# Performance work log

Measured on AMD Instinct MI355X. Metric: run time of the kernel, lower is better.

## Reference

```python
import jax, jax.numpy as jnp
import numpy as np

N_GRAPHS = 8192
NODES_PER = 32
H = 128
E = 524288
N = N_GRAPHS * NODES_PER


def setup_inputs() -> dict:
    key = jax.random.key(0)
    ks = jax.random.split(key, 20)
    feat = jax.random.normal(ks[0], (N, H), jnp.float32)
    # edges constrained within each session graph
    gid_e = jax.random.randint(ks[1], (E,), 0, N_GRAPHS)
    src = (gid_e * NODES_PER + jax.random.randint(ks[2], (E,), 0, NODES_PER)).astype(jnp.int32)
    dst = (gid_e * NODES_PER + jax.random.randint(ks[3], (E,), 0, NODES_PER)).astype(jnp.int32)
    cnt = jax.random.uniform(ks[4], (N,), jnp.float32, 1.0, 4.0)
    segment_ids = jnp.repeat(jnp.arange(N_GRAPHS, dtype=jnp.int32), NODES_PER)
    last_nodes = (jnp.arange(N_GRAPHS, dtype=jnp.int32) + 1) * NODES_PER - 1
    s = 1.0 / np.sqrt(H)
    u = lambda k, shape: jax.random.uniform(k, shape, jnp.float32, -s, s)
    return {
        'feat': feat, 'cnt': cnt,
        'W_in': u(ks[5], (H, H)), 'b_in': u(ks[6], (H,)),
        'W_og': u(ks[7], (H, H)), 'b_og': u(ks[8], (H,)),
        'W_ih': u(ks[9], (3 * H, 2 * H)), 'b_ih': u(ks[10], (3 * H,)),
        'W_hh': u(ks[11], (3 * H, H)), 'b_hh': u(ks[12], (3 * H,)),
        'W_u': u(ks[13], (H, H)),
        'W_v': u(ks[14], (H, H)), 'b_v': u(ks[15], (H,)),
        'w_e': u(ks[16], (H,)),
        'src': src, 'dst': dst, 'segment_ids': segment_ids, 'last_nodes': last_nodes,
    }


def reference(feat, cnt, W_in, b_in, W_og, b_og, W_ih, b_ih, W_hh, b_hh,
              W_u, W_v, b_v, w_e, src, dst, segment_ids, last_nodes):
    n = feat.shape[0]
    ones = jnp.ones(src.shape, jnp.float32)
    deg_in = jax.ops.segment_sum(ones, dst, num_segments=n)   # in-degree per node
    deg_out = jax.ops.segment_sum(ones, src, num_segments=n)  # out-degree per node
    # GGNN propagate (num_steps=1): copy_u_mean on g and on reversed g
    feat_in = feat @ W_in.T + b_in
    feat_out = feat @ W_og.T + b_og
    a_in = jax.ops.segment_sum(feat_in[src], dst, num_segments=n) / jnp.maximum(deg_in, 1.0)[:, None]
    a_out = jax.ops.segment_sum(feat_out[dst], src, num_segments=n) / jnp.maximum(deg_out, 1.0)[:, None]
    a = jnp.concatenate([a_in, a_out], axis=1)  # [N, 2H]
    # torch GRUCell
    gi = a @ W_ih.T + b_ih
    gh = feat @ W_hh.T + b_hh
    i_r, i_z, i_n = jnp.split(gi, 3, axis=1)
    h_r, h_z, h_n = jnp.split(gh, 3, axis=1)
    r = jax.nn.sigmoid(i_r + h_r)
    z = jax.nn.sigmoid(i_z + h_z)
    ng = jnp.tanh(i_n + r * h_n)
    hn = (1.0 - z) * ng + z * feat  # [N, H]
    # AttentionReadout
    feat_u = hn @ W_u.T
    feat_v = hn[last_nodes] @ W_v.T + b_v           # [B, H]
    e = jax.nn.sigmoid(feat_u + feat_v[segment_ids]) @ w_e  # [N]
    alpha = e * cnt
    ct_g = jax.ops.segment_sum(hn * alpha[:, None], segment_ids, num_segments=N_GRAPHS)
    ct_l = hn[last_nodes]
    return jnp.concatenate([ct_g, ct_l], axis=1)  # [B, 2H]
```

## Files before the change

### kernel.cpp

```cpp
#include <hip/hip_runtime.h>


#define NG    8192
#define NODES 32
#define HDIM  128
#define NEDGE 524288
#define NCONV 214272

typedef __bf16 bf16;
typedef __bf16 bf16x8 __attribute__((ext_vector_type(8)));
typedef float  f32x4  __attribute__((ext_vector_type(4)));
typedef unsigned int u32;
typedef unsigned char u8;

__device__ __forceinline__ f32x4 mfma16(bf16x8 a, bf16x8 b, f32x4 c) {
    return __builtin_amdgcn_mfma_f32_16x16x32_bf16(a, b, c, 0, 0, 0);
}

__device__ __forceinline__ float sigmoidf_(float x) { return 1.f / (1.f + __expf(-x)); }
__device__ __forceinline__ float tanhf_(float x) { return 1.f - 2.f / (__expf(2.f * x) + 1.f); }

__global__ __launch_bounds__(256) void k_prep(
        const u32* __restrict__ featw, u32* __restrict__ adjw,
        bf16* __restrict__ conv, u32* __restrict__ flagout,
        const void* t0, const void* t1, const void* t2,  const void* t3,
        const void* t4, const void* t5, const void* t6,  const void* t7,
        const void* t8, const void* t9, const void* t10, const void* t11) {
    const int b = blockIdx.x, tid = threadIdx.x;
    if (b < 2048) {
        int i = b * 1024 + tid * 4;
        *(uint4*)(adjw + i) = make_uint4(0u, 0u, 0u, 0u);
        return;
    }
    __shared__ int s_isf32;
    if (tid == 0) s_isf32 = 0;
    __syncthreads();
    {
        u32 hit = 0;
#pragma unroll
        for (int k = 0; k < 16; ++k) {
            u32 x = featw[tid * 16 + k];
            hit |= (((x >> 7) & 0xFFu) == 0xFFu) ? 1u : 0u;
        }
        if (hit) s_isf32 = 1;
    }
    __syncthreads();
    const bool isf32 = s_isf32 != 0;
    if (b == 2048 && tid == 0) *flagout = isf32 ? 1u : 0u;

    int e0 = (b - 2048) * 2048 + tid * 8;
    if (e0 >= NCONV) return;
    const int cnts[12] = {16384, 128, 16384, 128, 98304, 384, 49152, 384,
                          16384, 16384, 128, 128};
    int t = 0, base = 0;
    while (e0 >= base + cnts[t]) { base += cnts[t]; ++t; }
    int off = e0 - base;
    const void* sp;
    switch (t) {
        case 0: sp = t0; break; case 1: sp = t1; break;
        case 2: sp = t2; break; case 3: sp = t3; break;
        case 4: sp = t4; break; case 5: sp = t5; break;
        case 6: sp = t6; break; case 7: sp = t7; break;
        case 8: sp = t8; break; case 9: sp = t9; break;
        case 10: sp = t10; break; default: sp = t11; break;
    }
    if (isf32) {
        const float4* s = (const float4*)sp + (off >> 2);
        float4 a = s[0], bb = s[1];
        bf16x8 v;
        v[0] = (bf16)a.x;  v[1] = (bf16)a.y;  v[2] = (bf16)a.z;  v[3] = (bf16)a.w;
        v[4] = (bf16)bb.x; v[5] = (bf16)bb.y; v[6] = (bf16)bb.z; v[7] = (bf16)bb.w;
        *(bf16x8*)(conv + e0) = v;
    } else {
        *(uint4*)(conv + e0) = ((const uint4*)sp)[off >> 3];
    }
}

__global__ __launch_bounds__(256) void k_fuse(
        const bf16* __restrict__ W_in, const bf16* __restrict__ b_in,
        const bf16* __restrict__ W_og, const bf16* __restrict__ b_og,
        const bf16* __restrict__ W_ih, const bf16* __restrict__ b_ih,
        bf16* __restrict__ u_t, float* __restrict__ bw_in,
        float* __restrict__ bw_og) {
    const int jt = blockIdx.x;
    const int tid = threadIdx.x;
    const int wave = tid >> 6, lane = tid & 63, q = lane >> 4, c = lane & 15;
#pragma unroll 1
    for (int k2 = 0; k2 < 4; ++k2) {
        int kt = wave * 4 + k2;
        bool og = kt >= 8;
        const bf16* Wsrc = og ? W_og : W_in;
        int kcol = (kt & 7) * 16 + c;
        int mo = og ? 128 : 0;
        f32x4 acc = {0, 0, 0, 0};
#pragma unroll 1
        for (int t = 0; t < 4; ++t) {
            bf16x8 a = *(const bf16x8*)(W_ih + (jt * 16 + c) * 256 + mo + 32 * t + 8 * q);
            bf16x8 b;
#pragma unroll
            for (int jj = 0; jj < 8; ++jj)
                b[jj] = Wsrc[(32 * t + 8 * q + jj) * 128 + kcol];
            acc = mfma16(a, b, acc);
        }
#pragma unroll
        for (int r = 0; r < 4; ++r)
            u_t[(size_t)(jt * 16 + q * 4 + r) * 256 + kt * 16 + c] = (bf16)acc[r];
    }
    {
        int jj = tid >> 4, mm = tid & 15;
        int j = jt * 16 + jj;
        float si = 0.f, so = 0.f;
#pragma unroll
        for (int i = 0; i < 8; ++i) {
            int m = mm * 8 + i;
            si += (float)b_in[m] * (float)W_ih[j * 256 + m];
            so += (float)b_og[m] * (float)W_ih[j * 256 + 128 + m];
        }
        for (int m = 1; m < 16; m <<= 1) {
            si += __shfl_xor(si, m);
            so += __shfl_xor(so, m);
        }
        if (mm == 0) { bw_in[j] = si; bw_og[j] = so; }
    }
}

__global__ __launch_bounds__(256) void k_adj(const int* __restrict__ src,
                                             const int* __restrict__ dst,
                                             u32* __restrict__ adj) {
    int e = blockIdx.x * 256 + threadIdx.x;
    int s = src[e], d = dst[e];
    int g = s >> 5;
    u32 bidx = ((u32)g << 10) | ((u32)(d & 31) << 5) | (u32)(s & 31);
    atomicAdd(&adj[bidx >> 2], 1u << (8 * (bidx & 3)));
}

__global__ __launch_bounds__(512, 4) void k_mono(
        const void* __restrict__ featv, const void* __restrict__ cntv,
        const bf16* __restrict__ u_t,  const bf16* __restrict__ b_ih,
        const bf16* __restrict__ W_hh, const bf16* __restrict__ b_hh,
        const bf16* __restrict__ W_u,  const bf16* __restrict__ W_v,
        const bf16* __restrict__ b_v,  const bf16* __restrict__ w_e,
        const float* __restrict__ bw_in, const float* __restrict__ bw_og,
        const int* __restrict__ last_nodes, const u8* __restrict__ adj8,
        const u32* __restrict__ flag, float* __restrict__ out) {
    const int g2   = blockIdx.x;
    const int tid  = threadIdx.x;
    const int wave = tid >> 6, lane = tid & 63, q = lane >> 4, c = lane & 15;
    const bool isf32 = (*flag) != 0u;
    const int col  = wave * 16 + c;

    const int SF = 136;
    const int SC = 264;
    const int SA = 40;
    __shared__ __align__(16) bf16 s_feat[64 * 136];
    __shared__ __align__(16) bf16 s_fc  [64 * 264];
    __shared__ __align__(16) bf16 s_adjb[64 * 40];
    __shared__ __align__(16) bf16 s_adjT[64 * 40];
    __shared__ u32   s_adjw[512];
    __shared__ float s_invin[64], s_invout[64];
    __shared__ float s_din[64], s_dout[64];
    __shared__ float s_e[64], s_alpha[64];
    float* s_fv = (float*)s_adjw;

    if (isf32) {
        const float4* fp = (const float4*)((const float*)featv + (size_t)g2 * 8192);
        for (int ch = tid; ch < 2048; ch += 512) {
            float4 v = fp[ch];
            int row = ch >> 5, off = (ch & 31) * 4;
            bf16* dp = s_feat + row * SF + off;
            dp[0] = (bf16)v.x; dp[1] = (bf16)v.y; dp[2] = (bf16)v.z; dp[3] = (bf16)v.w;
        }
    } else {
        const uint4* fp = (const uint4*)((const bf16*)featv + (size_t)g2 * 8192);
        for (int ch = tid; ch < 1024; ch += 512) {
            int row = ch >> 4, off = (ch & 15) * 8;
            *(uint4*)(s_feat + row * SF + off) = fp[ch];
        }
    }
    s_adjw[tid] = ((const u32*)(adj8 + (size_t)g2 * 2048))[tid];
    if (tid < 64) s_e[tid] = 0.f;
    __syncthreads();

    {
        u32 w = s_adjw[tid];
        int vrow = tid >> 3;
        int grp  = tid >> 8;
        int vloc = vrow & 31;
        int u0 = (tid & 7) * 4;
#pragma unroll
        for (int j = 0; j < 4; ++j) {
            float cv = (float)((w >> (8 * j)) & 0xFFu);
            s_adjb[vrow * SA + u0 + j] = (bf16)cv;
            s_adjT[(grp * 32 + u0 + j) * SA + vloc] = (bf16)cv;
        }
    }
    if (tid < 64) {
        u32 s = 0;
        for (int i = 0; i < 8; ++i) {
            u32 w = s_adjw[tid * 8 + i];
            s += (w & 0xFF) + ((w >> 8) & 0xFF) + ((w >> 16) & 0xFF) + (w >> 24);
        }
        s_invin[tid] = 1.f / fmaxf((float)s, 1.f);
        s_din[tid] = (s > 0) ? 1.f : 0.f;
    } else if (tid < 128) {
        int uu = tid - 64; int grp = uu >> 5; int ul = uu & 31; u32 s = 0;
        for (int v = 0; v < 32; ++v)
            s += (s_adjw[grp * 256 + v * 8 + (ul >> 2)] >> (8 * (ul & 3))) & 0xFF;
        s_invout[uu] = 1.f / fmaxf((float)s, 1.f);
        s_dout[uu] = (s > 0) ? 1.f : 0.f;
    }
    f32x4 hnp[4] = {{0,0,0,0},{0,0,0,0},{0,0,0,0},{0,0,0,0}};
    {
        const bf16* Vp = W_hh + (256 + col) * HDIM;
#pragma unroll 1
        for (int t = 0; t < 4; ++t) {
            bf16x8 b = *(const bf16x8*)(Vp + 32 * t + 8 * q);
#pragma unroll
            for (int fr = 0; fr < 4; ++fr) {
                bf16x8 a = *(const bf16x8*)(s_feat + (fr * 16 + c) * SF + 32 * t + 8 * q);
                hnp[fr] = mfma16(a, b, hnp[fr]);
            }
        }
        float bh = (float)b_hh[256 + col];
#pragma unroll
        for (int fr = 0; fr < 4; ++fr)
#pragma unroll
            for (int r = 0; r < 4; ++r) hnp[fr][r] += bh;
    }
    __syncthreads();

#pragma unroll 1
    for (int kk = 0; kk < 2; ++kk) {
        int ct = wave * 2 + kk;
        int colb = (ct & 7) * 16;
        const bf16* Ab = (ct < 8) ? s_adjb : s_adjT;
        const float* inv = (ct < 8) ? s_invin : s_invout;
        bf16x8 bA, bB;
        const bf16* Bp0 = s_feat + (q * 8) * SF + colb + c;
        const bf16* Bp1 = s_feat + (32 + q * 8) * SF + colb + c;
#pragma unroll
        for (int jj = 0; jj < 8; ++jj) { bA[jj] = Bp0[jj * SF]; bB[jj] = Bp1[jj * SF]; }
        bf16x8 a0 = *(const bf16x8*)(Ab + c * SA + 8 * q);
        bf16x8 a1 = *(const bf16x8*)(Ab + (16 + c) * SA + 8 * q);
        bf16x8 a2 = *(const bf16x8*)(Ab + (32 + c) * SA + 8 * q);
        bf16x8 a3 = *(const bf16x8*)(Ab + (48 + c) * SA + 8 * q);
        f32x4 z = {0, 0, 0, 0};
        f32x4 p0 = mfma16(a0, bA, z);
        f32x4 p1 = mfma16(a1, bA, z);
        f32x4 p2 = mfma16(a2, bB, z);
        f32x4 p3 = mfma16(a3, bB, z);
#pragma unroll
        for (int r = 0; r < 4; ++r) {
            int r0 = q * 4 + r;
            s_fc[(r0)      * SC + ct * 16 + c] = (bf16)(p0[r] * inv[r0]);
            s_fc[(16 + r0) * SC + ct * 16 + c] = (bf16)(p1[r] * inv[16 + r0]);
            s_fc[(32 + r0) * SC + ct * 16 + c] = (bf16)(p2[r] * inv[32 + r0]);
            s_fc[(48 + r0) * SC + ct * 16 + c] = (bf16)(p3[r] * inv[48 + r0]);
        }
    }
    __syncthreads();

    f32x4 rr[4] = {{0,0,0,0},{0,0,0,0},{0,0,0,0},{0,0,0,0}};
    f32x4 zz[4] = {{0,0,0,0},{0,0,0,0},{0,0,0,0},{0,0,0,0}};
    f32x4 in_[4] = {{0,0,0,0},{0,0,0,0},{0,0,0,0},{0,0,0,0}};
    {
        const bf16* Ur = u_t + (size_t)(col) * 256;
        const bf16* Uz = u_t + (size_t)(128 + col) * 256;
        const bf16* Un = u_t + (size_t)(256 + col) * 256;
#pragma unroll 1
        for (int t = 0; t < 8; ++t) {
            bf16x8 br = *(const bf16x8*)(Ur + 32 * t + 8 * q);
            bf16x8 bz = *(const bf16x8*)(Uz + 32 * t + 8 * q);
            bf16x8 bn = *(const bf16x8*)(Un + 32 * t + 8 * q);
#pragma unroll
            for (int fr = 0; fr < 4; ++fr) {
                bf16x8 a = *(const bf16x8*)(s_fc + (fr * 16 + c) * SC + 32 * t + 8 * q);
                rr[fr] = mfma16(a, br, rr[fr]);
                zz[fr] = mfma16(a, bz, zz[fr]);
                in_[fr] = mfma16(a, bn, in_[fr]);
            }
        }
        const bf16* Vr = W_hh + (col) * HDIM;
        const bf16* Vz = W_hh + (128 + col) * HDIM;
#pragma unroll 1
        for (int t = 0; t < 4; ++t) {
            bf16x8 br = *(const bf16x8*)(Vr + 32 * t + 8 * q);
            bf16x8 bz = *(const bf16x8*)(Vz + 32 * t + 8 * q);
#pragma unroll
            for (int fr = 0; fr < 4; ++fr) {
                bf16x8 f = *(const bf16x8*)(s_feat + (fr * 16 + c) * SF + 32 * t + 8 * q);
                rr[fr] = mfma16(f, br, rr[fr]);
                zz[fr] = mfma16(f, bz, zz[fr]);
            }
        }
    }
    f32x4 hv[4];
    {
        float brz  = (float)b_ih[col]       + (float)b_hh[col];
        float bzz  = (float)b_ih[128 + col] + (float)b_hh[128 + col];
        float bin_ = (float)b_ih[256 + col];
        float bwr_i = bw_in[col],       bwr_o = bw_og[col];
        float bwz_i = bw_in[128 + col], bwz_o = bw_og[128 + col];
        float bwn_i = bw_in[256 + col], bwn_o = bw_og[256 + col];
#pragma unroll
        for (int fr = 0; fr < 4; ++fr) {
#pragma unroll
            for (int r = 0; r < 4; ++r) {
                int row = fr * 16 + q * 4 + r;
                float di = s_din[row], dou = s_dout[row];
                float rg = sigmoidf_(rr[fr][r] + brz + di * bwr_i + dou * bwr_o);
                float z_ = sigmoidf_(zz[fr][r] + bzz + di * bwz_i + dou * bwz_o);
                float ng = tanhf_(in_[fr][r] + bin_ + di * bwn_i + dou * bwn_o
                                  + rg * hnp[fr][r]);
                float fv = (float)s_feat[row * SF + col];
                hv[fr][r] = (1.f - z_) * ng + z_ * fv;
            }
        }
    }
    int llA = last_nodes[2 * g2] & 31;
    int llB = 32 + (last_nodes[2 * g2 + 1] & 31);
    __syncthreads();
#pragma unroll
    for (int fr = 0; fr < 4; ++fr)
#pragma unroll
        for (int r = 0; r < 4; ++r)
            s_feat[(fr * 16 + q * 4 + r) * SF + col] = (bf16)hv[fr][r];
    __syncthreads();
    const bf16* s_hn = s_feat;

#pragma unroll 1
    for (int gsel = 0; gsel < 2; ++gsel) {
        int ll = gsel ? llB : llA;
        const bf16* Ap = s_hn + ll * SF;
        const bf16* Wp = W_v + (size_t)col * HDIM;
        f32x4 acc = {0, 0, 0, 0};
#pragma unroll 1
        for (int t = 0; t < 4; ++t) {
            bf16x8 a = *(const bf16x8*)(Ap + 32 * t + 8 * q);
            bf16x8 b = *(const bf16x8*)(Wp + 32 * t + 8 * q);
            acc = mfma16(a, b, acc);
        }
        if (q == 0) s_fv[gsel * 128 + col] = acc[0] + (float)b_v[col];
    }
    __syncthreads();

    {
        const bf16* Wp = W_u + (size_t)col * HDIM;
        f32x4 ee[4] = {{0,0,0,0},{0,0,0,0},{0,0,0,0},{0,0,0,0}};
#pragma unroll 1
        for (int t = 0; t < 4; ++t) {
            bf16x8 b = *(const bf16x8*)(Wp + 32 * t + 8 * q);
#pragma unroll
            for (int fr = 0; fr < 4; ++fr) {
                bf16x8 a = *(const bf16x8*)(s_hn + (fr * 16 + c) * SF + 32 * t + 8 * q);
                ee[fr] = mfma16(a, b, ee[fr]);
            }
        }
        float we = (float)w_e[col];
        float fvA = s_fv[col], fvB = s_fv[128 + col];
#pragma unroll
        for (int fr = 0; fr < 4; ++fr) {
            float fv = (fr < 2) ? fvA : fvB;
#pragma unroll
            for (int r = 0; r < 4; ++r) {
                float v = sigmoidf_(ee[fr][r] + fv) * we;
                for (int m = 1; m < 16; m <<= 1) v += __shfl_xor(v, m);
                if (c == 0) atomicAdd(&s_e[fr * 16 + q * 4 + r], v);
            }
        }
    }
    __syncthreads();
    if (tid < 64) {
        float cv = isf32 ? ((const float*)cntv)[(size_t)g2 * 64 + tid]
                         : (float)((const bf16*)cntv)[(size_t)g2 * 64 + tid];
        s_alpha[tid] = s_e[tid] * cv;
    }
    __syncthreads();

    {
        int part = tid >> 7;
        int co = tid & 127;
        if (part == 0) {
            float s = 0.f;
#pragma unroll 4
            for (int n = 0; n < 32; ++n) s += s_alpha[n] * (float)s_hn[n * SF + co];
            out[(size_t)(2 * g2) * 256 + co] = s;
        } else if (part == 1) {
            out[(size_t)(2 * g2) * 256 + 128 + co] = (float)s_hn[llA * SF + co];
        } else if (part == 2) {
            float s = 0.f;
#pragma unroll 4
            for (int n = 32; n < 64; ++n) s += s_alpha[n] * (float)s_hn[n * SF + co];
            out[(size_t)(2 * g2 + 1) * 256 + co] = s;
        } else {
            out[(size_t)(2 * g2 + 1) * 256 + 128 + co] = (float)s_hn[llB * SF + co];
        }
    }
}

extern "C" void kernel_launch(void* const* d_in, const int* in_sizes, int n_in,
                              void* d_out, int out_size, void* d_ws, size_t ws_size,
                              hipStream_t stream) {
    const int* src  = (const int*)d_in[14];
    const int* dst  = (const int*)d_in[15];
    const int* last = (const int*)d_in[17];
    float* out = (float*)d_out;

    u32*  flag  = (u32*)d_ws;
    bf16* conv  = (bf16*)((char*)d_ws + 4096);
    float* bwin = (float*)((char*)d_ws + 430 * 1024);
    float* bwog = (float*)((char*)d_ws + 434 * 1024);
    bf16* u_t   = (bf16*)((char*)d_ws + 448 * 1024);
    u32*  adjw  = (u32*)((char*)d_ws + (1u << 20));
    const u8* adj8 = (const u8*)adjw;

    const int cnts[12] = {16384, 128, 16384, 128, 98304, 384, 49152, 384,
                          16384, 16384, 128, 128};
    bf16* cp[12];
    {
        bf16* p = conv;
        for (int i = 0; i < 12; ++i) { cp[i] = p; p += cnts[i]; }
    }

    k_prep<<<2048 + (NCONV + 2047) / 2048, 256, 0, stream>>>(
        (const u32*)d_in[0], adjw, conv, flag,
        d_in[2], d_in[3], d_in[4], d_in[5], d_in[6], d_in[7],
        d_in[8], d_in[9], d_in[10], d_in[11], d_in[12], d_in[13]);
    k_fuse<<<24, 256, 0, stream>>>(cp[0], cp[1], cp[2], cp[3], cp[4], cp[5],
                                   u_t, bwin, bwog);
    k_adj<<<NEDGE / 256, 256, 0, stream>>>(src, dst, adjw);
    k_mono<<<NG / 2, 512, 0, stream>>>(d_in[0], d_in[1],
                                       u_t, cp[5], cp[6], cp[7],
                                       cp[8], cp[9], cp[10], cp[11],
                                       bwin, bwog,
                                       last, adj8, flag, out);
}
```

Measured before the change: 483.3 us.

## Spill hn-gate to LDS, merge GRU loops, split fuse kernel, memset adjacency

Several changes at once. The hidden-gate accumulator (W_hh n-part) is now stored to shared memory as bf16 instead of being held in registers across the main GEMM, which reduces register pressure. The U and W_hh r/z MFMA loops are merged into one loop unrolled by 2. k_fuse is split into 96 blocks so each block handles one k-tile. The adjacency zeroing moves from k_prep blocks to hipMemsetAsync. The extra LDS (about 17KB per block) may reduce occupancy, and rounding h_n to bf16 slightly changes precision.

```diff
diff --git a/kernel.cpp b/kernel.cpp
--- a/kernel.cpp
+++ b/kernel.cpp
@@ -21,17 +21,12 @@
 __device__ __forceinline__ float tanhf_(float x) { return 1.f - 2.f / (__expf(2.f * x) + 1.f); }
 
 __global__ __launch_bounds__(256) void k_prep(
-        const u32* __restrict__ featw, u32* __restrict__ adjw,
+        const u32* __restrict__ featw,
         bf16* __restrict__ conv, u32* __restrict__ flagout,
         const void* t0, const void* t1, const void* t2,  const void* t3,
         const void* t4, const void* t5, const void* t6,  const void* t7,
         const void* t8, const void* t9, const void* t10, const void* t11) {
     const int b = blockIdx.x, tid = threadIdx.x;
-    if (b < 2048) {
-        int i = b * 1024 + tid * 4;
-        *(uint4*)(adjw + i) = make_uint4(0u, 0u, 0u, 0u);
-        return;
-    }
     __shared__ int s_isf32;
     if (tid == 0) s_isf32 = 0;
     __syncthreads();
@@ -46,9 +41,9 @@
     }
     __syncthreads();
     const bool isf32 = s_isf32 != 0;
-    if (b == 2048 && tid == 0) *flagout = isf32 ? 1u : 0u;
-
-    int e0 = (b - 2048) * 2048 + tid * 8;
+    if (b == 0 && tid == 0) *flagout = isf32 ? 1u : 0u;
+
+    int e0 = b * 2048 + tid * 8;
     if (e0 >= NCONV) return;
     const int cnts[12] = {16384, 128, 16384, 128, 98304, 384, 49152, 384,
                           16384, 16384, 128, 128};
@@ -82,12 +77,12 @@
         const bf16* __restrict__ W_ih, const bf16* __restrict__ b_ih,
         bf16* __restrict__ u_t, float* __restrict__ bw_in,
         float* __restrict__ bw_og) {
-    const int jt = blockIdx.x;
+    const int jt = blockIdx.x >> 2;
+    const int ksel = blockIdx.x & 3;
     const int tid = threadIdx.x;
     const int wave = tid >> 6, lane = tid & 63, q = lane >> 4, c = lane & 15;
-#pragma unroll 1
-    for (int k2 = 0; k2 < 4; ++k2) {
-        int kt = wave * 4 + k2;
+    {
+        int kt = wave * 4 + ksel;
         bool og = kt >= 8;
         const bf16* Wsrc = og ? W_og : W_in;
         int kcol = (kt & 7) * 16 + c;
@@ -106,7 +101,7 @@
         for (int r = 0; r < 4; ++r)
             u_t[(size_t)(jt * 16 + q * 4 + r) * 256 + kt * 16 + c] = (bf16)acc[r];
     }
-    {
+    if (ksel == 0) {
         int jj = tid >> 4, mm = tid & 15;
         int j = jt * 16 + jj;
         float si = 0.f, so = 0.f;
@@ -152,10 +147,12 @@
     const int SF = 136;
     const int SC = 264;
     const int SA = 40;
+    const int SH = 132;
     __shared__ __align__(16) bf16 s_feat[64 * 136];
     __shared__ __align__(16) bf16 s_fc  [64 * 264];
     __shared__ __align__(16) bf16 s_adjb[64 * 40];
     __shared__ __align__(16) bf16 s_adjT[64 * 40];
+    __shared__ __align__(16) bf16 s_hnp [64 * 132];
     __shared__ u32   s_adjw[512];
     __shared__ float s_invin[64], s_invout[64];
     __shared__ float s_din[64], s_dout[64];
@@ -209,8 +206,8 @@
         s_invout[uu] = 1.f / fmaxf((float)s, 1.f);
         s_dout[uu] = (s > 0) ? 1.f : 0.f;
     }
-    f32x4 hnp[4] = {{0,0,0,0},{0,0,0,0},{0,0,0,0},{0,0,0,0}};
-    {
+    {
+        f32x4 hp[4] = {{0,0,0,0},{0,0,0,0},{0,0,0,0},{0,0,0,0}};
         const bf16* Vp = W_hh + (256 + col) * HDIM;
 #pragma unroll 1
         for (int t = 0; t < 4; ++t) {
@@ -218,14 +215,15 @@
 #pragma unroll
             for (int fr = 0; fr < 4; ++fr) {
                 bf16x8 a = *(const bf16x8*)(s_feat + (fr * 16 + c) * SF + 32 * t + 8 * q);
-                hnp[fr] = mfma16(a, b, hnp[fr]);
+                hp[fr] = mfma16(a, b, hp[fr]);
             }
         }
         float bh = (float)b_hh[256 + col];
 #pragma unroll
         for (int fr = 0; fr < 4; ++fr)
 #pragma unroll
-            for (int r = 0; r < 4; ++r) hnp[fr][r] += bh;
+            for (int r = 0; r < 4; ++r)
+                s_hnp[(fr * 16 + q * 4 + r) * SH + col] = (bf16)(hp[fr][r] + bh);
     }
     __syncthreads();
 
@@ -267,7 +265,9 @@
         const bf16* Ur = u_t + (size_t)(col) * 256;
         const bf16* Uz = u_t + (size_t)(128 + col) * 256;
         const bf16* Un = u_t + (size_t)(256 + col) * 256;
-#pragma unroll 1
+        const bf16* Vr = W_hh + (col) * HDIM;
+        const bf16* Vz = W_hh + (128 + col) * HDIM;
+#pragma unroll 2
         for (int t = 0; t < 8; ++t) {
             bf16x8 br = *(const bf16x8*)(Ur + 32 * t + 8 * q);
             bf16x8 bz = *(const bf16x8*)(Uz + 32 * t + 8 * q);
@@ -279,18 +279,15 @@
                 zz[fr] = mfma16(a, bz, zz[fr]);
                 in_[fr] = mfma16(a, bn, in_[fr]);
             }
-        }
-        const bf16* Vr = W_hh + (col) * HDIM;
-        const bf16* Vz = W_hh + (128 + col) * HDIM;
-#pragma unroll 1
-        for (int t = 0; t < 4; ++t) {
-            bf16x8 br = *(const bf16x8*)(Vr + 32 * t + 8 * q);
-            bf16x8 bz = *(const bf16x8*)(Vz + 32 * t + 8 * q);
-#pragma unroll
-            for (int fr = 0; fr < 4; ++fr) {
-                bf16x8 f = *(const bf16x8*)(s_feat + (fr * 16 + c) * SF + 32 * t + 8 * q);
-                rr[fr] = mfma16(f, br, rr[fr]);
-                zz[fr] = mfma16(f, bz, zz[fr]);
+            if (t < 4) {
+                bf16x8 vr = *(const bf16x8*)(Vr + 32 * t + 8 * q);
+                bf16x8 vz = *(const bf16x8*)(Vz + 32 * t + 8 * q);
+#pragma unroll
+                for (int fr = 0; fr < 4; ++fr) {
+                    bf16x8 f = *(const bf16x8*)(s_feat + (fr * 16 + c) * SF + 32 * t + 8 * q);
+                    rr[fr] = mfma16(f, vr, rr[fr]);
+                    zz[fr] = mfma16(f, vz, zz[fr]);
+                }
             }
         }
     }
@@ -311,7 +308,7 @@
                 float rg = sigmoidf_(rr[fr][r] + brz + di * bwr_i + dou * bwr_o);
                 float z_ = sigmoidf_(zz[fr][r] + bzz + di * bwz_i + dou * bwz_o);
                 float ng = tanhf_(in_[fr][r] + bin_ + di * bwn_i + dou * bwn_o
-                                  + rg * hnp[fr][r]);
+                                  + rg * (float)s_hnp[row * SH + col]);
                 float fv = (float)s_feat[row * SF + col];
                 hv[fr][r] = (1.f - z_) * ng + z_ * fv;
             }
@@ -422,11 +419,12 @@
         for (int i = 0; i < 12; ++i) { cp[i] = p; p += cnts[i]; }
     }
 
-    k_prep<<<2048 + (NCONV + 2047) / 2048, 256, 0, stream>>>(
-        (const u32*)d_in[0], adjw, conv, flag,
+    hipMemsetAsync(adjw, 0, 8u << 20, stream);
+    k_prep<<<(NCONV + 2047) / 2048, 256, 0, stream>>>(
+        (const u32*)d_in[0], conv, flag,
         d_in[2], d_in[3], d_in[4], d_in[5], d_in[6], d_in[7],
         d_in[8], d_in[9], d_in[10], d_in[11], d_in[12], d_in[13]);
-    k_fuse<<<24, 256, 0, stream>>>(cp[0], cp[1], cp[2], cp[3], cp[4], cp[5],
+    k_fuse<<<96, 256, 0, stream>>>(cp[0], cp[1], cp[2], cp[3], cp[4], cp[5],
                                    u_t, bwin, bwog);
     k_adj<<<NEDGE / 256, 256, 0, stream>>>(src, dst, adjw);
     k_mono<<<NG / 2, 512, 0, stream>>>(d_in[0], d_in[1],
```

Result: no change. 481.6 us (-0.4%).
